# Kernel optimization log

Hardware: AMD Instinct MI355X
Metric: run time of the kernel (lower is better)

## Reference

```python
import jax, jax.numpy as jnp
import numpy as np

EMBEDDING = 1024
PARAMETERS = 4096

def setup_inputs() -> dict:
    key = jax.random.key(0)
    kx, kK, kV = jax.random.split(key, 3)
    x = jax.random.normal(kx, (4, 2048, EMBEDDING), dtype=jnp.float32)
    K = jax.random.normal(kK, (PARAMETERS, EMBEDDING), dtype=jnp.float32)
    V = jax.random.normal(kV, (PARAMETERS, EMBEDDING), dtype=jnp.float32)
    return {"x": x, "K": K, "V": V}

def reference(x, K, V):
    # scores: [b, s, p] = scale * x @ K.T
    scale = EMBEDDING ** (-0.5)
    scores = scale * jnp.einsum('bse,pe->bsp', x, K)
    attn = jax.nn.softmax(scores, axis=-1)
    # out: [b, s, e] = attn @ V
    return jnp.einsum('bsp,pe->bse', attn, V)
```

## Files before the change

### kernel.cpp

```cpp
#include <hip/hip_runtime.h>
#include <hip/hip_bf16.h>

typedef __bf16 bf16x8 __attribute__((ext_vector_type(8)));
typedef __bf16 bf16x4 __attribute__((ext_vector_type(4)));
typedef float floatx4 __attribute__((ext_vector_type(4)));

__device__ __forceinline__ void async16(void* lds, const void* g) {
  __builtin_amdgcn_global_load_lds(
      (const __attribute__((address_space(1))) unsigned int*)g,
      (__attribute__((address_space(3))) unsigned int*)lds, 16, 0, 0);
}

__global__ __launch_bounds__(256) void preprocess_kernel(
    const float* __restrict__ x, const float* __restrict__ Kp,
    const float* __restrict__ V, __bf16* __restrict__ xb,
    __bf16* __restrict__ Kb, __bf16* __restrict__ Vt,
    float* __restrict__ lsum) {
  const int b = blockIdx.x;
  const int t = threadIdx.x;
  if (b < 2048) {
#pragma unroll
    for (int k = 0; k < 4; ++k) {
      const int i = b * 1024 + k * 256 + t;
      float4 v = ((const float4*)x)[i];
      bf16x4 o = {(__bf16)v.x, (__bf16)v.y, (__bf16)v.z, (__bf16)v.w};
      ((bf16x4*)xb)[i] = o;
    }
  } else if (b < 3072) {
#pragma unroll
    for (int k = 0; k < 4; ++k) {
      const int i = (b - 2048) * 1024 + k * 256 + t;
      float4 v = ((const float4*)Kp)[i];
      bf16x4 o = {(__bf16)v.x, (__bf16)v.y, (__bf16)v.z, (__bf16)v.w};
      ((bf16x4*)Kb)[i] = o;
    }
  } else if (b < 4096) {
    __shared__ float tile[64][65];
    const int bb = b - 3072;
    const int bx = bb & 63, by = bb >> 6;
    for (int i = t; i < 64 * 64; i += 256) {
      const int r = i >> 6, c = i & 63;
      tile[r][c] = V[(size_t)(bx * 64 + r) * 1024 + by * 64 + c];
    }
    __syncthreads();
    for (int i = t; i < 64 * 64; i += 256) {
      const int r = i >> 6, c = i & 63;
      Vt[(size_t)(by * 64 + r) * 4096 + bx * 64 + c] = (__bf16)tile[c][r];
    }
  } else {
#pragma unroll
    for (int k = 0; k < 8; ++k)
      ((floatx4*)lsum)[k * 256 + t] = floatx4{0.f, 0.f, 0.f, 0.f};
  }
}

template <int MODE, int KS, int NS>
__global__ __launch_bounds__(256) void gemm_kernel(const __bf16* __restrict__ A,
                                                   const __bf16* __restrict__ B,
                                                   __bf16* __restrict__ Cb,
                                                   float* __restrict__ Cf,
                                                   float* __restrict__ lsum) {
  constexpr int BK = 64;
  __shared__ __bf16 As[128 * BK];
  __shared__ __bf16 Bs[128 * BK];
  const int t = threadIdx.x;
  const int lane = t & 63;
  const int w = t >> 6;
  const int wr = w >> 1, wc = w & 1;

  const int id = blockIdx.x;
  const int g = id & 7;
  const int s = id >> 3;
  const int mt = g * 8 + (s & 7);
  const int nt = s >> 3;
  const int m0 = mt * 128;
  const int n0 = nt * 128;

  const __bf16* Ab = A + (size_t)m0 * KS;
  const __bf16* Bb = B + (size_t)n0 * KS;

  floatx4 acc[4][4] = {};

  const int mA = t >> 3;
  const int qs = (t & 7) ^ (mA & 7);
  const __bf16* aP = Ab + (size_t)mA * KS + qs * 8;
  const __bf16* bP = Bb + (size_t)mA * KS + qs * 8;
  char* dA = (char*)As + t * 16;
  char* dB = (char*)Bs + t * 16;

  const int rl = lane & 15;
  const int qq = lane >> 4;
  const int fo = rl * 128 + ((qq ^ (rl & 7)) << 4);

  for (int k0 = 0; k0 < KS; k0 += BK) {
#pragma unroll
    for (int r = 0; r < 4; ++r) {
      async16(dA + r * 4096, aP + (size_t)r * 32 * KS + k0);
      async16(dB + r * 4096, bP + (size_t)r * 32 * KS + k0);
    }
    __syncthreads();

    bf16x8 aF[4], bF[4];
#pragma unroll
    for (int i = 0; i < 4; ++i) {
      aF[i] = *(const bf16x8*)((const char*)As + wr * 8192 + i * 2048 + fo);
      bF[i] = *(const bf16x8*)((const char*)Bs + wc * 8192 + i * 2048 + fo);
    }
#pragma unroll
    for (int i = 0; i < 4; ++i)
#pragma unroll
      for (int j = 0; j < 4; ++j)
        acc[i][j] = __builtin_amdgcn_mfma_f32_16x16x32_bf16(aF[i], bF[j], acc[i][j], 0, 0, 0);
#pragma unroll
    for (int i = 0; i < 4; ++i) {
      aF[i] = *(const bf16x8*)((const char*)As + wr * 8192 + i * 2048 + (fo ^ 64));
      bF[i] = *(const bf16x8*)((const char*)Bs + wc * 8192 + i * 2048 + (fo ^ 64));
    }
#pragma unroll
    for (int i = 0; i < 4; ++i)
#pragma unroll
      for (int j = 0; j < 4; ++j)
        acc[i][j] = __builtin_amdgcn_mfma_f32_16x16x32_bf16(aF[i], bF[j], acc[i][j], 0, 0, 0);
    __syncthreads();
  }

  const int cm = wr * 64 + ((lane >> 4) << 2);
  const int cn = wc * 64 + (lane & 15);
  if (MODE == 0) {
#pragma unroll
    for (int i = 0; i < 4; ++i)
#pragma unroll
      for (int r = 0; r < 4; ++r) {
        const int m = m0 + cm + i * 16 + r;
        float rs = 0.f;
#pragma unroll
        for (int j = 0; j < 4; ++j) {
          const float e = __expf(fminf(acc[i][j][r] * 0.03125f, 30.0f));
          rs += e;
          Cb[(size_t)m * NS + n0 + cn + j * 16] = (__bf16)e;
        }
        rs += __shfl_xor(rs, 1, 64);
        rs += __shfl_xor(rs, 2, 64);
        rs += __shfl_xor(rs, 4, 64);
        rs += __shfl_xor(rs, 8, 64);
        if ((lane & 15) == 0) atomicAdd(&lsum[m], rs);
      }
  } else {
#pragma unroll
    for (int i = 0; i < 4; ++i)
#pragma unroll
      for (int r = 0; r < 4; ++r) {
        const int m = m0 + cm + i * 16 + r;
        const float inv = 1.0f / lsum[m];
#pragma unroll
        for (int j = 0; j < 4; ++j)
          Cf[(size_t)m * NS + n0 + cn + j * 16] = acc[i][j][r] * inv;
      }
  }
}

extern "C" void kernel_launch(void* const* d_in, const int* in_sizes, int n_in,
                              void* d_out, int out_size, void* d_ws, size_t ws_size,
                              hipStream_t stream) {
  const float* x = (const float*)d_in[0];
  const float* K = (const float*)d_in[1];
  const float* V = (const float*)d_in[2];
  float* out = (float*)d_out;

  char* ws = (char*)d_ws;
  __bf16* xb = (__bf16*)ws;
  __bf16* Kb = (__bf16*)(ws + (16u << 20));
  __bf16* Vt = (__bf16*)(ws + (24u << 20));
  __bf16* P  = (__bf16*)(ws + (32u << 20));
  float*  l  = (float*)(ws + (96u << 20));

  preprocess_kernel<<<4097, 256, 0, stream>>>(x, K, V, xb, Kb, Vt, l);
  gemm_kernel<0, 1024, 4096><<<2048, 256, 0, stream>>>(xb, Kb, P, nullptr, l);
  gemm_kernel<1, 4096, 1024><<<512, 256, 0, stream>>>(P, Vt, nullptr, out, l);
}
```

Baseline: 257.4 us.

## Use 256x128 tiles with 512 threads and triple-buffered async LDS pipeline

The GEMM kernel moves to 512-thread blocks computing 256x128 output tiles, with a three-stage LDS ring buffer filled by async global-to-LDS loads two iterations ahead. Each K step is split into two MFMA phases interleaved with the prefetch issue, using explicit waitcnt, barriers, sched_barrier and setprio to overlap memory with compute. The aim is to hide global load latency and raise reuse per block, at the cost of 144KB of LDS per block, which limits occupancy. The correctness of the hand-placed waitcnt counts is a risk.

```diff
diff --git a/kernel.cpp b/kernel.cpp
--- a/kernel.cpp
+++ b/kernel.cpp
@@ -55,73 +55,124 @@
 }
 
 template <int MODE, int KS, int NS>
-__global__ __launch_bounds__(256) void gemm_kernel(const __bf16* __restrict__ A,
-                                                   const __bf16* __restrict__ B,
-                                                   __bf16* __restrict__ Cb,
-                                                   float* __restrict__ Cf,
-                                                   float* __restrict__ lsum) {
+__global__ __launch_bounds__(512, 2) void gemm_kernel(const __bf16* __restrict__ A,
+                                                      const __bf16* __restrict__ B,
+                                                      __bf16* __restrict__ Cb,
+                                                      float* __restrict__ Cf,
+                                                      float* __restrict__ lsum) {
   constexpr int BK = 64;
-  __shared__ __bf16 As[128 * BK];
-  __shared__ __bf16 Bs[128 * BK];
+  constexpr int NT = KS / BK;
+  constexpr int NNT = NS / 128;
+  __shared__ char lds[147456];
+
   const int t = threadIdx.x;
   const int lane = t & 63;
   const int w = t >> 6;
-  const int wr = w >> 1, wc = w & 1;
+  const int wr = w >> 1;
+  const int wc = w & 1;
 
   const int id = blockIdx.x;
   const int g = id & 7;
   const int s = id >> 3;
-  const int mt = g * 8 + (s & 7);
-  const int nt = s >> 3;
-  const int m0 = mt * 128;
+  const int mt = g * 4 + s / NNT;
+  const int nt = s % NNT;
+  const int m0 = mt * 256;
   const int n0 = nt * 128;
 
-  const __bf16* Ab = A + (size_t)m0 * KS;
-  const __bf16* Bb = B + (size_t)n0 * KS;
-
-  floatx4 acc[4][4] = {};
-
-  const int mA = t >> 3;
-  const int qs = (t & 7) ^ (mA & 7);
-  const __bf16* aP = Ab + (size_t)mA * KS + qs * 8;
-  const __bf16* bP = Bb + (size_t)mA * KS + qs * 8;
-  char* dA = (char*)As + t * 16;
-  char* dB = (char*)Bs + t * 16;
+  const int rowT = t >> 3;
+  const int cg = (t & 7) ^ (rowT & 7);
+  const __bf16* aS = A + (size_t)(m0 + rowT) * KS + cg * 8;
+  const __bf16* bS = B + (size_t)(n0 + rowT) * KS + cg * 8;
+  const int dT = t * 16;
 
   const int rl = lane & 15;
   const int qq = lane >> 4;
   const int fo = rl * 128 + ((qq ^ (rl & 7)) << 4);
-
-  for (int k0 = 0; k0 < KS; k0 += BK) {
-#pragma unroll
-    for (int r = 0; r < 4; ++r) {
-      async16(dA + r * 4096, aP + (size_t)r * 32 * KS + k0);
-      async16(dB + r * 4096, bP + (size_t)r * 32 * KS + k0);
-    }
-    __syncthreads();
-
-    bf16x8 aF[4], bF[4];
+  const int aBase = wr * 8192 + fo;
+  const int bBase = 32768 + wc * 8192 + fo;
+
+  floatx4 acc[4][4] = {};
+
+#pragma unroll
+  for (int s2 = 0; s2 < 4; ++s2)
+    async16(lds + s2 * 8192 + dT, aS + (size_t)s2 * 64 * KS);
+#pragma unroll
+  for (int s2 = 0; s2 < 2; ++s2)
+    async16(lds + 32768 + s2 * 8192 + dT, bS + (size_t)s2 * 64 * KS);
+#pragma unroll
+  for (int s2 = 0; s2 < 4; ++s2)
+    async16(lds + 49152 + s2 * 8192 + dT, aS + (size_t)s2 * 64 * KS + BK);
+#pragma unroll
+  for (int s2 = 0; s2 < 2; ++s2)
+    async16(lds + 49152 + 32768 + s2 * 8192 + dT, bS + (size_t)s2 * 64 * KS + BK);
+  asm volatile("s_waitcnt vmcnt(6)" ::: "memory");
+  __builtin_amdgcn_s_barrier();
+
+  unsigned o0 = 0, o1 = 49152, o2 = 98304;
+
+  for (int T = 0; T < NT; ++T) {
+    const bool pf = (T + 2) < NT;
+    const int kpf = (T + 2) * BK;
+
+    bf16x8 aF[4][2], bF[4][2];
 #pragma unroll
     for (int i = 0; i < 4; ++i) {
-      aF[i] = *(const bf16x8*)((const char*)As + wr * 8192 + i * 2048 + fo);
-      bF[i] = *(const bf16x8*)((const char*)Bs + wc * 8192 + i * 2048 + fo);
-    }
-#pragma unroll
-    for (int i = 0; i < 4; ++i)
-#pragma unroll
-      for (int j = 0; j < 4; ++j)
-        acc[i][j] = __builtin_amdgcn_mfma_f32_16x16x32_bf16(aF[i], bF[j], acc[i][j], 0, 0, 0);
-#pragma unroll
-    for (int i = 0; i < 4; ++i) {
-      aF[i] = *(const bf16x8*)((const char*)As + wr * 8192 + i * 2048 + (fo ^ 64));
-      bF[i] = *(const bf16x8*)((const char*)Bs + wc * 8192 + i * 2048 + (fo ^ 64));
-    }
-#pragma unroll
-    for (int i = 0; i < 4; ++i)
-#pragma unroll
-      for (int j = 0; j < 4; ++j)
-        acc[i][j] = __builtin_amdgcn_mfma_f32_16x16x32_bf16(aF[i], bF[j], acc[i][j], 0, 0, 0);
-    __syncthreads();
+      aF[i][0] = *(const bf16x8*)(lds + o0 + aBase + i * 2048);
+      aF[i][1] = *(const bf16x8*)(lds + o0 + ((aBase + i * 2048) ^ 64));
+    }
+#pragma unroll
+    for (int j = 0; j < 2; ++j) {
+      bF[j][0] = *(const bf16x8*)(lds + o0 + bBase + j * 2048);
+      bF[j][1] = *(const bf16x8*)(lds + o0 + ((bBase + j * 2048) ^ 64));
+    }
+    if (pf) {
+#pragma unroll
+      for (int s2 = 0; s2 < 3; ++s2)
+        async16(lds + o2 + s2 * 8192 + dT, aS + (size_t)s2 * 64 * KS + kpf);
+    }
+    __builtin_amdgcn_s_barrier();
+    asm volatile("s_waitcnt lgkmcnt(0)" ::: "memory");
+    __builtin_amdgcn_sched_barrier(0);
+    __builtin_amdgcn_s_setprio(1);
+#pragma unroll
+    for (int ks = 0; ks < 2; ++ks)
+#pragma unroll
+      for (int i = 0; i < 4; ++i)
+#pragma unroll
+        for (int j = 0; j < 2; ++j)
+          acc[i][j] = __builtin_amdgcn_mfma_f32_16x16x32_bf16(aF[i][ks], bF[j][ks], acc[i][j], 0, 0, 0);
+    __builtin_amdgcn_s_setprio(0);
+    __builtin_amdgcn_s_barrier();
+
+#pragma unroll
+    for (int j = 2; j < 4; ++j) {
+      bF[j][0] = *(const bf16x8*)(lds + o0 + bBase + j * 2048);
+      bF[j][1] = *(const bf16x8*)(lds + o0 + ((bBase + j * 2048) ^ 64));
+    }
+    if (pf) {
+      async16(lds + o2 + 3 * 8192 + dT, aS + (size_t)3 * 64 * KS + kpf);
+#pragma unroll
+      for (int s2 = 0; s2 < 2; ++s2)
+        async16(lds + o2 + 32768 + s2 * 8192 + dT, bS + (size_t)s2 * 64 * KS + kpf);
+      asm volatile("s_waitcnt vmcnt(6)" ::: "memory");
+    } else {
+      asm volatile("s_waitcnt vmcnt(0)" ::: "memory");
+    }
+    __builtin_amdgcn_s_barrier();
+    asm volatile("s_waitcnt lgkmcnt(0)" ::: "memory");
+    __builtin_amdgcn_sched_barrier(0);
+    __builtin_amdgcn_s_setprio(1);
+#pragma unroll
+    for (int ks = 0; ks < 2; ++ks)
+#pragma unroll
+      for (int i = 0; i < 4; ++i)
+#pragma unroll
+        for (int j = 2; j < 4; ++j)
+          acc[i][j] = __builtin_amdgcn_mfma_f32_16x16x32_bf16(aF[i][ks], bF[j][ks], acc[i][j], 0, 0, 0);
+    __builtin_amdgcn_s_setprio(0);
+    __builtin_amdgcn_s_barrier();
+
+    const unsigned tmp = o0; o0 = o1; o1 = o2; o2 = tmp;
   }
 
   const int cm = wr * 64 + ((lane >> 4) << 2);
@@ -175,6 +226,6 @@
   float*  l  = (float*)(ws + (96u << 20));
 
   preprocess_kernel<<<4097, 256, 0, stream>>>(x, K, V, xb, Kb, Vt, l);
-  gemm_kernel<0, 1024, 4096><<<2048, 256, 0, stream>>>(xb, Kb, P, nullptr, l);
-  gemm_kernel<1, 4096, 1024><<<512, 256, 0, stream>>>(P, Vt, nullptr, out, l);
-}
+  gemm_kernel<0, 1024, 4096><<<1024, 512, 0, stream>>>(xb, Kb, P, nullptr, l);
+  gemm_kernel<1, 4096, 1024><<<256, 512, 0, stream>>>(P, Vt, nullptr, out, l);
+}
```

Result: slower. 279.1 us (+8.4%).

## Rewrite GEMMs as 256x256 tiles with pipelined LDS staging and split-K

Applied to the files above, without the earlier changes.

Both GEMMs move from 128x128 tiles with 256 threads to 256x256 tiles with 512 threads. K-slices are double-buffered in 128KB of LDS, with global loads issued ahead of the MFMA phases, explicit vmcnt waits, barriers and setprio. The second GEMM is split along K into two parts that accumulate into the output with float atomics, so the preprocess kernel now also zeroes the output. The aim is more data reuse per tile, overlap of loads with MFMA work, and better occupancy for the small second GEMM, at the cost of atomic traffic and one extra pass to zero the output.

```diff
diff --git a/kernel.cpp b/kernel.cpp
--- a/kernel.cpp
+++ b/kernel.cpp
@@ -15,7 +15,7 @@
     const float* __restrict__ x, const float* __restrict__ Kp,
     const float* __restrict__ V, __bf16* __restrict__ xb,
     __bf16* __restrict__ Kb, __bf16* __restrict__ Vt,
-    float* __restrict__ lsum) {
+    float* __restrict__ lsum, float* __restrict__ outz) {
   const int b = blockIdx.x;
   const int t = threadIdx.x;
   if (b < 2048) {
@@ -47,97 +47,165 @@
       const int r = i >> 6, c = i & 63;
       Vt[(size_t)(by * 64 + r) * 4096 + bx * 64 + c] = (__bf16)tile[c][r];
     }
-  } else {
+  } else if (b == 4096) {
 #pragma unroll
     for (int k = 0; k < 8; ++k)
       ((floatx4*)lsum)[k * 256 + t] = floatx4{0.f, 0.f, 0.f, 0.f};
+  } else {
+    const size_t bb = b - 4097;
+#pragma unroll
+    for (int k = 0; k < 4; ++k)
+      ((float4*)outz)[bb * 1024 + k * 256 + t] = float4{0.f, 0.f, 0.f, 0.f};
   }
 }
 
-template <int MODE, int KS, int NS>
-__global__ __launch_bounds__(256) void gemm_kernel(const __bf16* __restrict__ A,
-                                                   const __bf16* __restrict__ B,
-                                                   __bf16* __restrict__ Cb,
-                                                   float* __restrict__ Cf,
-                                                   float* __restrict__ lsum) {
-  constexpr int BK = 64;
-  __shared__ __bf16 As[128 * BK];
-  __shared__ __bf16 Bs[128 * BK];
+template <int MODE, int LD, int KR, int NS, int MTX, int SPL>
+__global__ __launch_bounds__(512, 2) void gemm_kernel(const __bf16* __restrict__ A,
+                                                      const __bf16* __restrict__ B,
+                                                      __bf16* __restrict__ Cb,
+                                                      float* __restrict__ Cf,
+                                                      float* __restrict__ lsum) {
+  constexpr int NT = KR / 64;
+  __shared__ char lds[131072];
+
   const int t = threadIdx.x;
   const int lane = t & 63;
   const int w = t >> 6;
-  const int wr = w >> 1, wc = w & 1;
+  const int wm = w >> 2;
+  const int wn = w & 3;
 
   const int id = blockIdx.x;
   const int g = id & 7;
   const int s = id >> 3;
-  const int mt = g * 8 + (s & 7);
-  const int nt = s >> 3;
-  const int m0 = mt * 128;
-  const int n0 = nt * 128;
-
-  const __bf16* Ab = A + (size_t)m0 * KS;
-  const __bf16* Bb = B + (size_t)n0 * KS;
-
-  floatx4 acc[4][4] = {};
-
-  const int mA = t >> 3;
-  const int qs = (t & 7) ^ (mA & 7);
-  const __bf16* aP = Ab + (size_t)mA * KS + qs * 8;
-  const __bf16* bP = Bb + (size_t)mA * KS + qs * 8;
-  char* dA = (char*)As + t * 16;
-  char* dB = (char*)Bs + t * 16;
+  const int ks = s % SPL;
+  const int r2 = s / SPL;
+  const int mt = g * MTX + (r2 % MTX);
+  const int nt = r2 / MTX;
+  const int m0 = mt * 256;
+  const int n0 = nt * 256;
+  const size_t koff = (size_t)ks * KR;
+
+  const int v = (t & 7) ^ ((t >> 3) & 7);
+  const int srow = 2 * (t >> 3) + (v >> 2);
+  const int sk8 = (v & 3) * 8;
+  const __bf16* aS = A + (size_t)(m0 + srow) * LD + koff + sk8;
+  const __bf16* bS = B + (size_t)(n0 + srow) * LD + koff + sk8;
+  const int t16 = t * 16;
+
+  auto stageA = [&](int slot, int kElem) {
+    const __bf16* p = aS + kElem;
+    async16(lds + slot + t16, p);
+    async16(lds + slot + 8192 + t16, p + (size_t)128 * LD);
+  };
+  auto stageB = [&](int slot, int kElem) {
+    const __bf16* p = bS + kElem;
+    async16(lds + slot + t16, p);
+    async16(lds + slot + 8192 + t16, p + (size_t)128 * LD);
+  };
 
   const int rl = lane & 15;
   const int qq = lane >> 4;
-  const int fo = rl * 128 + ((qq ^ (rl & 7)) << 4);
-
-  for (int k0 = 0; k0 < KS; k0 += BK) {
-#pragma unroll
-    for (int r = 0; r < 4; ++r) {
-      async16(dA + r * 4096, aP + (size_t)r * 32 * KS + k0);
-      async16(dB + r * 4096, bP + (size_t)r * 32 * KS + k0);
-    }
-    __syncthreads();
-
+  const int fo = (rl >> 1) * 128 + (((((rl & 1) << 2) | qq) ^ (rl >> 1)) << 4);
+  const int aOff = wm * 8192 + fo;
+  const int bOff = wn * 4096 + fo;
+
+  floatx4 acc[8][4] = {};
+
+  stageA(0, 0);          stageB(32768, 0);
+  stageA(16384, 32);     stageB(49152, 32);
+  stageA(65536, 64);     stageB(98304, 64);
+  asm volatile("s_waitcnt vmcnt(8)" ::: "memory");
+  __builtin_amdgcn_s_barrier();
+
+  for (int T = 0; T < NT; ++T) {
+    const int bas = (T & 1) << 16;
+    const int oth = bas ^ 65536;
+    const int kT = T * 64;
     bf16x8 aF[4], bF[4];
-#pragma unroll
-    for (int i = 0; i < 4; ++i) {
-      aF[i] = *(const bf16x8*)((const char*)As + wr * 8192 + i * 2048 + fo);
-      bF[i] = *(const bf16x8*)((const char*)Bs + wc * 8192 + i * 2048 + fo);
-    }
+
+#pragma unroll
+    for (int i = 0; i < 4; ++i) aF[i] = *(const bf16x8*)(lds + bas + aOff + i * 1024);
+#pragma unroll
+    for (int j = 0; j < 4; ++j) bF[j] = *(const bf16x8*)(lds + bas + 32768 + bOff + j * 1024);
+    if (T + 1 < NT) stageA(oth + 16384, kT + 96);
+    __builtin_amdgcn_s_barrier();
+    asm volatile("s_waitcnt lgkmcnt(0)" ::: "memory");
+    __builtin_amdgcn_sched_barrier(0);
+    __builtin_amdgcn_s_setprio(1);
 #pragma unroll
     for (int i = 0; i < 4; ++i)
 #pragma unroll
       for (int j = 0; j < 4; ++j)
         acc[i][j] = __builtin_amdgcn_mfma_f32_16x16x32_bf16(aF[i], bF[j], acc[i][j], 0, 0, 0);
-#pragma unroll
-    for (int i = 0; i < 4; ++i) {
-      aF[i] = *(const bf16x8*)((const char*)As + wr * 8192 + i * 2048 + (fo ^ 64));
-      bF[i] = *(const bf16x8*)((const char*)Bs + wc * 8192 + i * 2048 + (fo ^ 64));
-    }
+    __builtin_amdgcn_s_setprio(0);
+    __builtin_amdgcn_s_barrier();
+
+#pragma unroll
+    for (int i = 0; i < 4; ++i) aF[i] = *(const bf16x8*)(lds + bas + aOff + 4096 + i * 1024);
+    if (T + 1 < NT) stageB(oth + 49152, kT + 96);
+    if (T == NT - 1) asm volatile("s_waitcnt vmcnt(0)" ::: "memory");
+    else             asm volatile("s_waitcnt vmcnt(8)" ::: "memory");
+    __builtin_amdgcn_s_barrier();
+    asm volatile("s_waitcnt lgkmcnt(0)" ::: "memory");
+    __builtin_amdgcn_sched_barrier(0);
+    __builtin_amdgcn_s_setprio(1);
+#pragma unroll
+    for (int i = 0; i < 4; ++i)
+#pragma unroll
+      for (int j = 0; j < 4; ++j)
+        acc[4 + i][j] = __builtin_amdgcn_mfma_f32_16x16x32_bf16(aF[i], bF[j], acc[4 + i][j], 0, 0, 0);
+    __builtin_amdgcn_s_setprio(0);
+    __builtin_amdgcn_s_barrier();
+
+#pragma unroll
+    for (int i = 0; i < 4; ++i) aF[i] = *(const bf16x8*)(lds + bas + 16384 + aOff + i * 1024);
+#pragma unroll
+    for (int j = 0; j < 4; ++j) bF[j] = *(const bf16x8*)(lds + bas + 49152 + bOff + j * 1024);
+    if (T + 2 < NT) stageA(bas, kT + 128);
+    __builtin_amdgcn_s_barrier();
+    asm volatile("s_waitcnt lgkmcnt(0)" ::: "memory");
+    __builtin_amdgcn_sched_barrier(0);
+    __builtin_amdgcn_s_setprio(1);
 #pragma unroll
     for (int i = 0; i < 4; ++i)
 #pragma unroll
       for (int j = 0; j < 4; ++j)
         acc[i][j] = __builtin_amdgcn_mfma_f32_16x16x32_bf16(aF[i], bF[j], acc[i][j], 0, 0, 0);
-    __syncthreads();
+    __builtin_amdgcn_s_setprio(0);
+    __builtin_amdgcn_s_barrier();
+
+#pragma unroll
+    for (int i = 0; i < 4; ++i) aF[i] = *(const bf16x8*)(lds + bas + 16384 + aOff + 4096 + i * 1024);
+    if (T + 2 < NT) stageB(bas + 32768, kT + 128);
+    if (T + 2 < NT)      asm volatile("s_waitcnt vmcnt(8)" ::: "memory");
+    else if (T + 1 < NT) asm volatile("s_waitcnt vmcnt(4)" ::: "memory");
+    __builtin_amdgcn_s_barrier();
+    asm volatile("s_waitcnt lgkmcnt(0)" ::: "memory");
+    __builtin_amdgcn_sched_barrier(0);
+    __builtin_amdgcn_s_setprio(1);
+#pragma unroll
+    for (int i = 0; i < 4; ++i)
+#pragma unroll
+      for (int j = 0; j < 4; ++j)
+        acc[4 + i][j] = __builtin_amdgcn_mfma_f32_16x16x32_bf16(aF[i], bF[j], acc[4 + i][j], 0, 0, 0);
+    __builtin_amdgcn_s_setprio(0);
+    __builtin_amdgcn_s_barrier();
   }
 
-  const int cm = wr * 64 + ((lane >> 4) << 2);
-  const int cn = wc * 64 + (lane & 15);
+  const int cmB = wm * 128 + ((lane >> 4) << 2);
+  const int cn = n0 + wn * 64 + (lane & 15);
   if (MODE == 0) {
 #pragma unroll
-    for (int i = 0; i < 4; ++i)
+    for (int i = 0; i < 8; ++i)
 #pragma unroll
       for (int r = 0; r < 4; ++r) {
-        const int m = m0 + cm + i * 16 + r;
+        const int m = m0 + cmB + i * 16 + r;
         float rs = 0.f;
 #pragma unroll
         for (int j = 0; j < 4; ++j) {
           const float e = __expf(fminf(acc[i][j][r] * 0.03125f, 30.0f));
           rs += e;
-          Cb[(size_t)m * NS + n0 + cn + j * 16] = (__bf16)e;
+          Cb[(size_t)m * NS + cn + j * 16] = (__bf16)e;
         }
         rs += __shfl_xor(rs, 1, 64);
         rs += __shfl_xor(rs, 2, 64);
@@ -147,14 +215,14 @@
       }
   } else {
 #pragma unroll
-    for (int i = 0; i < 4; ++i)
+    for (int i = 0; i < 8; ++i)
 #pragma unroll
       for (int r = 0; r < 4; ++r) {
-        const int m = m0 + cm + i * 16 + r;
+        const int m = m0 + cmB + i * 16 + r;
         const float inv = 1.0f / lsum[m];
 #pragma unroll
         for (int j = 0; j < 4; ++j)
-          Cf[(size_t)m * NS + n0 + cn + j * 16] = acc[i][j][r] * inv;
+          atomicAdd(&Cf[(size_t)m * NS + cn + j * 16], acc[i][j][r] * inv);
       }
   }
 }
@@ -174,7 +242,7 @@
   __bf16* P  = (__bf16*)(ws + (32u << 20));
   float*  l  = (float*)(ws + (96u << 20));
 
-  preprocess_kernel<<<4097, 256, 0, stream>>>(x, K, V, xb, Kb, Vt, l);
-  gemm_kernel<0, 1024, 4096><<<2048, 256, 0, stream>>>(xb, Kb, P, nullptr, l);
-  gemm_kernel<1, 4096, 1024><<<512, 256, 0, stream>>>(P, Vt, nullptr, out, l);
-}
+  preprocess_kernel<<<6145, 256, 0, stream>>>(x, K, V, xb, Kb, Vt, l, out);
+  gemm_kernel<0, 1024, 1024, 4096, 4, 1><<<512, 512, 0, stream>>>(xb, Kb, P, nullptr, l);
+  gemm_kernel<1, 4096, 2048, 1024, 4, 2><<<256, 512, 0, stream>>>(P, Vt, nullptr, out, l);
+}
```

Result: slower. 290.0 us (+12.7%).
